# Performance work log

Measured on AMD Instinct MI355X. Metric: run time of the kernel, lower is better.

The kernel has to match this reference:

```python
import jax, jax.numpy as jnp
import numpy as np

S, L, B = 64, 64, 16
D_IN, D_ATTN = 1024, 512


def setup_inputs() -> dict:
    key = jax.random.key(0)
    ks = jax.random.split(key, 8)
    context = jax.random.normal(ks[0], (S, L, B, D_IN), dtype=jnp.float32)
    query = jax.random.normal(ks[1], (L, B, D_IN), dtype=jnp.float32)
    mask = jnp.ones((S, L, B), dtype=jnp.int32)
    # Linear params (torch layout: weight [out, in], bias [out])
    sc = 1.0 / np.sqrt(D_IN)
    Wc = jax.random.uniform(ks[2], (D_ATTN, D_IN), minval=-sc, maxval=sc, dtype=jnp.float32)
    bc = jax.random.uniform(ks[3], (D_ATTN,), minval=-sc, maxval=sc, dtype=jnp.float32)
    Wq = jax.random.uniform(ks[4], (D_ATTN, D_IN), minval=-sc, maxval=sc, dtype=jnp.float32)
    bq = jax.random.uniform(ks[5], (D_ATTN,), minval=-sc, maxval=sc, dtype=jnp.float32)
    v = jax.random.uniform(ks[6], (D_ATTN,), dtype=jnp.float32)  # torch.rand -> U[0,1)
    return {"context": context, "query": query, "mask": mask,
            "Wc": Wc, "bc": bc, "Wq": Wq, "bq": bq, "v": v}


def reference(context, query, mask, Wc, bc, Wq, bq, v):
    # context: [s,l,b,din], query: [l,b,din]
    context_proj = jnp.einsum('slbi,di->slbd', context, Wc) + bc  # [s,l,b,da]
    query_proj = jnp.einsum('lbi,di->lbd', query, Wq) + bq        # [l,b,da]
    scores = jnp.tanh(context_proj + query_proj[None])            # [s,l,b,da]
    scores = jnp.einsum('slbd,d->slb', scores, v)                 # [s,l,b]
    scores = jnp.where(mask == 0, jnp.float32(-1e9), scores)
    alpha = jax.nn.softmax(scores, axis=0)                        # softmax over s
    attn_output = jnp.einsum('slb,slbd->lbd', alpha, context)     # [l,b,din]
    return (attn_output, alpha)
```

## Files before the change

kernel.cpp:

```cpp
#include <hip/hip_runtime.h>
#include <hip/hip_fp16.h>
#include <stdint.h>

#define S_DIM 64
#define L_DIM 64
#define B_DIM 16
#define LB    1024
#define DIN   1024
#define DA    512
#define M_TOT 65536

#define BM 128
#define BN 512
#define BK 64
#define NT (DIN / BK)

using f16x8 = __attribute__((ext_vector_type(8))) _Float16;
using f32x4 = __attribute__((ext_vector_type(4))) float;

typedef const __attribute__((address_space(1))) void* gas_ptr;
typedef __attribute__((address_space(3))) void* las_ptr;

__device__ __forceinline__ void load_lds16(const void* g, void* l) {
    __builtin_amdgcn_global_load_lds((gas_ptr)g, (las_ptr)l, 16, 0, 0);
}

__device__ __forceinline__ float fast_tanh(float x) {
    return 1.0f - 2.0f / (__expf(2.0f * x) + 1.0f);
}

__global__ void cvt_all(const float* __restrict__ Wc, const float* __restrict__ Wq,
                        const float* __restrict__ q,
                        _Float16* __restrict__ Wch, _Float16* __restrict__ Wqh,
                        _Float16* __restrict__ Qh) {
    int i = blockIdx.x * 256 + threadIdx.x;
    if (i < DA * DIN)            Wch[i] = (_Float16)Wc[i];
    else if (i < 2 * DA * DIN)   Wqh[i - DA * DIN] = (_Float16)Wq[i - DA * DIN];
    else                         Qh[i - 2 * DA * DIN] = (_Float16)q[i - 2 * DA * DIN];
}

__global__ __launch_bounds__(256) void qp_gemm(
    const _Float16* __restrict__ Qh,
    const _Float16* __restrict__ Wqh,
    const float* __restrict__ bq, const float* __restrict__ bc,
    float* __restrict__ qp)
{
    __shared__ __align__(16) _Float16 lA[64 * 64];
    __shared__ __align__(16) _Float16 lB[64 * 64];
    const int t = threadIdx.x;
    const int w = t >> 6, lane = t & 63;
    const int quad = lane >> 4, m16 = lane & 15;
    const int n0 = blockIdx.x * 64, lb0 = blockIdx.y * 64;

    f32x4 acc[4] = {};

    for (int kt = 0; kt < DIN / 64; ++kt) {
#pragma unroll
        for (int i = 0; i < 2; ++i) {
            int c = (w * 2 + i) * 64 + lane;
            int row = c >> 3;
            int kc = (c & 7) ^ (row & 7);
            load_lds16(Qh  + (size_t)(lb0 + row) * DIN + kt * 64 + kc * 8, (char*)lA + (size_t)c * 16);
            load_lds16(Wqh + (size_t)(n0  + row) * DIN + kt * 64 + kc * 8, (char*)lB + (size_t)c * 16);
        }
        __syncthreads();
#pragma unroll
        for (int kk = 0; kk < 64; kk += 32) {
            int cq = (kk >> 3) + quad;
            int ar = 16 * w + m16;
            f16x8 a = *(const f16x8*)((const char*)lA + ar * 128 + ((cq ^ (ar & 7)) * 16));
#pragma unroll
            for (int j = 0; j < 4; ++j) {
                int br = 16 * j + m16;
                f16x8 b = *(const f16x8*)((const char*)lB + br * 128 + ((cq ^ (br & 7)) * 16));
                acc[j] = __builtin_amdgcn_mfma_f32_16x16x32_f16(a, b, acc[j], 0, 0, 0);
            }
        }
        __syncthreads();
    }
#pragma unroll
    for (int j = 0; j < 4; ++j) {
        int n = n0 + 16 * j + m16;
        float bias = bq[n] + bc[n];
#pragma unroll
        for (int r = 0; r < 4; ++r) {
            int lb = lb0 + 16 * w + quad * 4 + r;
            qp[(size_t)lb * DA + n] = acc[j][r] + bias;
        }
    }
}

__global__ __launch_bounds__(512, 2) void score_gemm4(
    const float* __restrict__ ctx,
    const _Float16* __restrict__ Wch,
    const float* __restrict__ qp,
    const float* __restrict__ v,
    _Float16* __restrict__ ctxh,
    float* __restrict__ sc)
{
    __shared__ __align__(16) _Float16 lA[BM * BK];
    __shared__ __align__(16) _Float16 lB[2][BN * BK];
    __shared__ float lP[4][BM];

    const int t = threadIdx.x;
    const int w = t >> 6, lane = t & 63;
    const int quad = lane >> 4, m16 = lane & 15;
    const int wm = w & 1, wn = w >> 1;

    int bid = blockIdx.x;
    int mb = (bid & 7) * 64 + (bid >> 3);
    const int m0 = mb * BM;
    const int lb0 = m0 & (LB - 1);

    const int arow = t >> 2;
    const int c0   = (t & 3) * 2;

    auto stageB = [&](int kt, int buf) {
#pragma unroll
        for (int i = 0; i < 8; ++i) {
            int c = (w * 8 + i) * 64 + lane;
            int row = c >> 3;
            int kc = (c & 7) ^ (row & 7);
            load_lds16(Wch + (size_t)row * DIN + kt * BK + kc * 8,
                       (char*)lB[buf] + (size_t)c * 16);
        }
    };

    f32x4 pf[4];
    auto issueA = [&](int kt) {
        const float* p = ctx + (size_t)(m0 + arow) * DIN + kt * BK + c0 * 8;
        pf[0] = *(const f32x4*)(p);
        pf[1] = *(const f32x4*)(p + 4);
        pf[2] = *(const f32x4*)(p + 8);
        pf[3] = *(const f32x4*)(p + 12);
    };

    stageB(0, 0);
    issueA(0);

    f32x4 acc[4][8];
#pragma unroll
    for (int i = 0; i < 4; ++i) {
        int rl = lb0 + wm * 64 + 16 * i + quad * 4;
#pragma unroll
        for (int j = 0; j < 8; ++j) {
            int n = wn * 128 + 16 * j + m16;
#pragma unroll
            for (int r = 0; r < 4; ++r)
                acc[i][j][r] = qp[(size_t)(rl + r) * DA + n];
        }
    }

    asm volatile("s_waitcnt vmcnt(0)" ::: "memory");
    __builtin_amdgcn_s_barrier();
    __builtin_amdgcn_sched_barrier(0);

    for (int kt = 0; kt < NT; ++kt) {
        const int cur = kt & 1;

        f16x8 h0 = {(_Float16)pf[0][0], (_Float16)pf[0][1], (_Float16)pf[0][2], (_Float16)pf[0][3],
                    (_Float16)pf[1][0], (_Float16)pf[1][1], (_Float16)pf[1][2], (_Float16)pf[1][3]};
        f16x8 h1 = {(_Float16)pf[2][0], (_Float16)pf[2][1], (_Float16)pf[2][2], (_Float16)pf[2][3],
                    (_Float16)pf[3][0], (_Float16)pf[3][1], (_Float16)pf[3][2], (_Float16)pf[3][3]};
        *(f16x8*)((char*)lA + arow * 128 + (((c0)     ^ (arow & 7)) * 16)) = h0;
        *(f16x8*)((char*)lA + arow * 128 + (((c0 + 1) ^ (arow & 7)) * 16)) = h1;
        _Float16* cd = ctxh + (size_t)(m0 + arow) * DIN + kt * BK + c0 * 8;
        *(f16x8*)cd = h0;
        *(f16x8*)(cd + 8) = h1;

        if (kt + 1 < NT) { stageB(kt + 1, cur ^ 1); issueA(kt + 1); }

        asm volatile("s_waitcnt lgkmcnt(0)" ::: "memory");
        __builtin_amdgcn_s_barrier();
        __builtin_amdgcn_sched_barrier(0);

#pragma unroll
        for (int kk2 = 0; kk2 < 2; ++kk2) {
            int cq = kk2 * 4 + quad;
            f16x8 a[4], b[8];
#pragma unroll
            for (int i = 0; i < 4; ++i) {
                int ar = wm * 64 + 16 * i + m16;
                a[i] = *(const f16x8*)((const char*)lA + ar * 128 + ((cq ^ (ar & 7)) * 16));
            }
#pragma unroll
            for (int j = 0; j < 8; ++j) {
                int br = wn * 128 + 16 * j + m16;
                b[j] = *(const f16x8*)((const char*)lB[cur] + br * 128 + ((cq ^ (br & 7)) * 16));
            }
            __builtin_amdgcn_s_setprio(1);
#pragma unroll
            for (int i = 0; i < 4; ++i)
#pragma unroll
                for (int j = 0; j < 8; ++j)
                    acc[i][j] = __builtin_amdgcn_mfma_f32_16x16x32_f16(a[i], b[j], acc[i][j], 0, 0, 0);
            __builtin_amdgcn_s_setprio(0);
        }

        asm volatile("s_waitcnt vmcnt(0)" ::: "memory");
        __builtin_amdgcn_s_barrier();
        __builtin_amdgcn_sched_barrier(0);
    }

    float vv[8];
#pragma unroll
    for (int j = 0; j < 8; ++j) vv[j] = v[wn * 128 + 16 * j + m16];

    float part[16];
#pragma unroll
    for (int i = 0; i < 4; ++i)
#pragma unroll
        for (int r = 0; r < 4; ++r) {
            float s = 0.f;
#pragma unroll
            for (int j = 0; j < 8; ++j)
                s += fast_tanh(acc[i][j][r]) * vv[j];
            part[i * 4 + r] = s;
        }
#pragma unroll
    for (int off = 1; off < 16; off <<= 1) {
#pragma unroll
        for (int k = 0; k < 16; ++k) part[k] += __shfl_xor(part[k], off, 64);
    }
    if (m16 == 0) {
#pragma unroll
        for (int k = 0; k < 16; ++k) {
            int rl = wm * 64 + 16 * (k >> 2) + quad * 4 + (k & 3);
            lP[wn][rl] = part[k];
        }
    }
    __syncthreads();
    if (t < BM) {
        float s = lP[0][t] + lP[1][t] + lP[2][t] + lP[3][t];
        sc[m0 + t] = s;
    }
}

__global__ __launch_bounds__(256, 3) void score_gemm(
    const float* __restrict__ ctx, const _Float16* __restrict__ Wch,
    const float* __restrict__ qp, const float* __restrict__ v,
    float* __restrict__ scores)
{
    __shared__ __align__(16) _Float16 lA[128 * 64];
    __shared__ __align__(16) _Float16 lB[128 * 64];
    __shared__ float lP[2][128];

    const int t = threadIdx.x;
    const int w = t >> 6, lane = t & 63;
    const int quad = lane >> 4, m16 = lane & 15;
    const int wm = w & 1, wn = w >> 1;

    int bid = blockIdx.x;
    int xcd = bid & 7;
    int j2 = bid >> 3;
    int nqf = j2 & 3;
    int mbf = ((j2 >> 2) << 3) | xcd;
    const int m0 = mbf * 128;
    const int n0 = nqf * 128;

    f32x4 acc[4][4] = {};

    const int arow = t >> 1;
    const int akc4 = (t & 1) * 4;
    const float* gA = ctx + (size_t)(m0 + arow) * DIN + (t & 1) * 32;

    for (int kt = 0; kt < DIN / 64; ++kt) {
        {
            const float* p = gA + kt * 64;
            f32x4 f[8];
#pragma unroll
            for (int qd = 0; qd < 8; ++qd) f[qd] = *(const f32x4*)(p + qd * 4);
#pragma unroll
            for (int q2 = 0; q2 < 4; ++q2) {
                f16x8 h = {(_Float16)f[2*q2][0], (_Float16)f[2*q2][1],
                           (_Float16)f[2*q2][2], (_Float16)f[2*q2][3],
                           (_Float16)f[2*q2+1][0], (_Float16)f[2*q2+1][1],
                           (_Float16)f[2*q2+1][2], (_Float16)f[2*q2+1][3]};
                int c = akc4 + q2;
                *(f16x8*)((char*)lA + arow * 128 + ((c ^ (arow & 7)) * 16)) = h;
            }
        }
#pragma unroll
        for (int i = 0; i < 4; ++i) {
            int c = (w * 4 + i) * 64 + lane;
            int row = c >> 3;
            int kc = (c & 7) ^ (row & 7);
            load_lds16(Wch + (size_t)(n0 + row) * DIN + kt * 64 + kc * 8, (char*)lB + (size_t)c * 16);
        }
        __syncthreads();
#pragma unroll
        for (int kk = 0; kk < 64; kk += 32) {
            int cq = (kk >> 3) + quad;
            f16x8 a[4], b[4];
#pragma unroll
            for (int i = 0; i < 4; ++i) {
                int ar = wm * 64 + 16 * i + m16;
                a[i] = *(const f16x8*)((const char*)lA + ar * 128 + ((cq ^ (ar & 7)) * 16));
            }
#pragma unroll
            for (int j = 0; j < 4; ++j) {
                int br = wn * 64 + 16 * j + m16;
                b[j] = *(const f16x8*)((const char*)lB + br * 128 + ((cq ^ (br & 7)) * 16));
            }
#pragma unroll
            for (int i = 0; i < 4; ++i)
#pragma unroll
                for (int j = 0; j < 4; ++j)
                    acc[i][j] = __builtin_amdgcn_mfma_f32_16x16x32_f16(a[i], b[j], acc[i][j], 0, 0, 0);
        }
        __syncthreads();
    }

    float vv[4];
    int nn[4];
#pragma unroll
    for (int j = 0; j < 4; ++j) { nn[j] = n0 + wn * 64 + 16 * j + m16; vv[j] = v[nn[j]]; }

    float part[16];
#pragma unroll
    for (int i = 0; i < 4; ++i) {
#pragma unroll
        for (int r = 0; r < 4; ++r) {
            int gm = m0 + wm * 64 + 16 * i + quad * 4 + r;
            int lb = gm & (LB - 1);
            float s = 0.f;
#pragma unroll
            for (int j = 0; j < 4; ++j) {
                float x = acc[i][j][r] + qp[(size_t)lb * DA + nn[j]];
                s += fast_tanh(x) * vv[j];
            }
            part[i * 4 + r] = s;
        }
    }
#pragma unroll
    for (int off = 1; off < 16; off <<= 1) {
#pragma unroll
        for (int k = 0; k < 16; ++k) part[k] += __shfl_xor(part[k], off, 64);
    }
    if (m16 == 0) {
#pragma unroll
        for (int k = 0; k < 16; ++k) {
            int row_local = wm * 64 + 16 * (k >> 2) + quad * 4 + (k & 3);
            lP[wn][row_local] = part[k];
        }
    }
    __syncthreads();
    if (t < 128) {
        float s = lP[0][t] + lP[1][t];
        atomicAdd(&scores[m0 + t], s);
    }
}

__global__ __launch_bounds__(64) void softmax2(const float* __restrict__ scores,
                                               const int* __restrict__ mask,
                                               float* __restrict__ alpha) {
    int lb = blockIdx.x;
    int s = threadIdx.x;
    float x = scores[s * LB + lb];
    if (mask[s * LB + lb] == 0) x = -1e9f;
    float mx = x;
#pragma unroll
    for (int off = 1; off < 64; off <<= 1) mx = fmaxf(mx, __shfl_xor(mx, off, 64));
    float e = __expf(x - mx);
    float sum = e;
#pragma unroll
    for (int off = 1; off < 64; off <<= 1) sum += __shfl_xor(sum, off, 64);
    alpha[s * LB + lb] = e / sum;
}

__global__ __launch_bounds__(128) void weighted_sum2(
    const _Float16* __restrict__ ctxh, const float* __restrict__ alpha,
    float* __restrict__ out) {
    __shared__ float lAl[S_DIM];
    const int lb = blockIdx.x;
    const int t = threadIdx.x;
    if (t < S_DIM) lAl[t] = alpha[t * LB + lb];
    __syncthreads();
    float acc[8] = {};
    const _Float16* base = ctxh + (size_t)lb * DIN + t * 8;
#pragma unroll 8
    for (int s = 0; s < S_DIM; ++s) {
        float a = lAl[s];
        f16x8 c = *(const f16x8*)(base + (size_t)s * LB * DIN);
#pragma unroll
        for (int j = 0; j < 8; ++j) acc[j] += a * (float)c[j];
    }
    f32x4 lo = {acc[0], acc[1], acc[2], acc[3]};
    f32x4 hi = {acc[4], acc[5], acc[6], acc[7]};
    *(f32x4*)(out + (size_t)lb * DIN + t * 8) = lo;
    *(f32x4*)(out + (size_t)lb * DIN + t * 8 + 4) = hi;
}

__global__ __launch_bounds__(256) void weighted_sum(
    const float* __restrict__ ctx, const float* __restrict__ alpha,
    float* __restrict__ out) {
    __shared__ float lAl[S_DIM];
    const int lb = blockIdx.x;
    const int t = threadIdx.x;
    if (t < S_DIM) lAl[t] = alpha[t * LB + lb];
    __syncthreads();
    f32x4 acc = {0.f, 0.f, 0.f, 0.f};
    const float* base = ctx + (size_t)lb * DIN + t * 4;
#pragma unroll 4
    for (int s = 0; s < S_DIM; ++s) {
        float a = lAl[s];
        f32x4 c = *(const f32x4*)(base + (size_t)s * LB * DIN);
        acc += a * c;
    }
    *(f32x4*)(out + (size_t)lb * DIN + t * 4) = acc;
}

extern "C" void kernel_launch(void* const* d_in, const int* in_sizes, int n_in,
                              void* d_out, int out_size, void* d_ws, size_t ws_size,
                              hipStream_t stream) {
    (void)in_sizes; (void)n_in; (void)out_size;
    const float* ctx   = (const float*)d_in[0];
    const float* query = (const float*)d_in[1];
    const int*   mask  = (const int*)d_in[2];
    const float* Wc    = (const float*)d_in[3];
    const float* bc    = (const float*)d_in[4];
    const float* Wq    = (const float*)d_in[5];
    const float* bq    = (const float*)d_in[6];
    const float* v     = (const float*)d_in[7];

    float* out_attn  = (float*)d_out;
    float* out_alpha = (float*)d_out + (size_t)LB * DIN;

    char* ws = (char*)d_ws;
    _Float16* Wch = (_Float16*)(ws);
    _Float16* Wqh = (_Float16*)(ws + (1 << 20));
    _Float16* Qh  = (_Float16*)(ws + (2 << 20));
    float*    qp  = (float*)(ws + (4 << 20));
    float*    sc  = (float*)(ws + (6 << 20));
    _Float16* ctxh = (_Float16*)(ws + (8 << 20));

    const size_t need = (size_t)(8 + 128) << 20;
    const bool bigws = ws_size >= need;

    cvt_all<<<(2 * DA * DIN + LB * DIN) / 256, 256, 0, stream>>>(Wc, Wq, query, Wch, Wqh, Qh);
    qp_gemm<<<dim3(DA / 64, LB / 64), 256, 0, stream>>>(Qh, Wqh, bq, bc, qp);

    if (bigws) {
        score_gemm4<<<M_TOT / BM, 512, 0, stream>>>(ctx, Wch, qp, v, ctxh, sc);
        softmax2<<<LB, 64, 0, stream>>>(sc, mask, out_alpha);
        weighted_sum2<<<LB, 128, 0, stream>>>(ctxh, out_alpha, out_attn);
    } else {
        hipMemsetAsync(sc, 0, (size_t)M_TOT * sizeof(float), stream);
        score_gemm<<<2048, 256, 0, stream>>>(ctx, Wch, qp, v, sc);
        softmax2<<<LB, 64, 0, stream>>>(sc, mask, out_alpha);
        weighted_sum<<<LB, 256, 0, stream>>>(ctx, out_alpha, out_attn);
    }
}
```

Measured before the change: 483.4 us.

## Split score GEMM across two N-halves with single-buffered B for higher occupancy

The fused score GEMM now tiles N at 256 instead of 512, so each block handles half of the attention dimension and the grid doubles. It writes two partial score arrays that a new softmax kernel sums. B is single-buffered and loaded each iteration, with vmcnt-based waits replacing the full drain, and launch bounds request more waves per CU. Only one of each block pair writes the fp16 context copy. The cost is that the context A tile is read and converted twice, and the B load is no longer prefetched a step ahead, which may expose latency.

```diff
diff --git a/kernel.cpp b/kernel.cpp
--- a/kernel.cpp
+++ b/kernel.cpp
@@ -11,7 +11,7 @@
 #define M_TOT 65536
 
 #define BM 128
-#define BN 512
+#define BN 256
 #define BK 64
 #define NT (DIN / BK)
 
@@ -90,7 +90,7 @@
     }
 }
 
-__global__ __launch_bounds__(512, 2) void score_gemm4(
+__global__ __launch_bounds__(512, 6) void score_gemm5(
     const float* __restrict__ ctx,
     const _Float16* __restrict__ Wch,
     const float* __restrict__ qp,
@@ -99,7 +99,7 @@
     float* __restrict__ sc)
 {
     __shared__ __align__(16) _Float16 lA[BM * BK];
-    __shared__ __align__(16) _Float16 lB[2][BN * BK];
+    __shared__ __align__(16) _Float16 lB[BN * BK];
     __shared__ float lP[4][BM];
 
     const int t = threadIdx.x;
@@ -108,21 +108,26 @@
     const int wm = w & 1, wn = w >> 1;
 
     int bid = blockIdx.x;
-    int mb = (bid & 7) * 64 + (bid >> 3);
+    int xcd = bid & 7;
+    int idx = bid >> 3;
+    const int nq = idx & 1;
+    const int mb = xcd * 64 + (idx >> 1);
     const int m0 = mb * BM;
+    const int n0 = nq * BN;
     const int lb0 = m0 & (LB - 1);
+    const bool wr_ctxh = (nq == 0);
 
     const int arow = t >> 2;
     const int c0   = (t & 3) * 2;
 
-    auto stageB = [&](int kt, int buf) {
-#pragma unroll
-        for (int i = 0; i < 8; ++i) {
-            int c = (w * 8 + i) * 64 + lane;
+    auto stageB = [&](int kt) {
+#pragma unroll
+        for (int i = 0; i < 4; ++i) {
+            int c = (w * 4 + i) * 64 + lane;
             int row = c >> 3;
             int kc = (c & 7) ^ (row & 7);
-            load_lds16(Wch + (size_t)row * DIN + kt * BK + kc * 8,
-                       (char*)lB[buf] + (size_t)c * 16);
+            load_lds16(Wch + (size_t)(n0 + row) * DIN + kt * BK + kc * 8,
+                       (char*)lB + (size_t)c * 16);
         }
     };
 
@@ -135,28 +140,23 @@
         pf[3] = *(const f32x4*)(p + 12);
     };
 
-    stageB(0, 0);
     issueA(0);
 
-    f32x4 acc[4][8];
+    f32x4 acc[4][4];
 #pragma unroll
     for (int i = 0; i < 4; ++i) {
         int rl = lb0 + wm * 64 + 16 * i + quad * 4;
 #pragma unroll
-        for (int j = 0; j < 8; ++j) {
-            int n = wn * 128 + 16 * j + m16;
+        for (int j = 0; j < 4; ++j) {
+            int n = n0 + wn * 64 + 16 * j + m16;
 #pragma unroll
             for (int r = 0; r < 4; ++r)
                 acc[i][j][r] = qp[(size_t)(rl + r) * DA + n];
         }
     }
 
-    asm volatile("s_waitcnt vmcnt(0)" ::: "memory");
-    __builtin_amdgcn_s_barrier();
-    __builtin_amdgcn_sched_barrier(0);
-
     for (int kt = 0; kt < NT; ++kt) {
-        const int cur = kt & 1;
+        stageB(kt);
 
         f16x8 h0 = {(_Float16)pf[0][0], (_Float16)pf[0][1], (_Float16)pf[0][2], (_Float16)pf[0][3],
                     (_Float16)pf[1][0], (_Float16)pf[1][1], (_Float16)pf[1][2], (_Float16)pf[1][3]};
@@ -164,12 +164,16 @@
                     (_Float16)pf[3][0], (_Float16)pf[3][1], (_Float16)pf[3][2], (_Float16)pf[3][3]};
         *(f16x8*)((char*)lA + arow * 128 + (((c0)     ^ (arow & 7)) * 16)) = h0;
         *(f16x8*)((char*)lA + arow * 128 + (((c0 + 1) ^ (arow & 7)) * 16)) = h1;
-        _Float16* cd = ctxh + (size_t)(m0 + arow) * DIN + kt * BK + c0 * 8;
-        *(f16x8*)cd = h0;
-        *(f16x8*)(cd + 8) = h1;
-
-        if (kt + 1 < NT) { stageB(kt + 1, cur ^ 1); issueA(kt + 1); }
-
+        if (wr_ctxh) {
+            _Float16* cd = ctxh + (size_t)(m0 + arow) * DIN + kt * BK + c0 * 8;
+            *(f16x8*)cd = h0;
+            *(f16x8*)(cd + 8) = h1;
+        }
+
+        issueA(kt + 1 < NT ? kt + 1 : NT - 1);
+
+        if (wr_ctxh) asm volatile("s_waitcnt vmcnt(6)" ::: "memory");
+        else         asm volatile("s_waitcnt vmcnt(4)" ::: "memory");
         asm volatile("s_waitcnt lgkmcnt(0)" ::: "memory");
         __builtin_amdgcn_s_barrier();
         __builtin_amdgcn_sched_barrier(0);
@@ -177,34 +181,34 @@
 #pragma unroll
         for (int kk2 = 0; kk2 < 2; ++kk2) {
             int cq = kk2 * 4 + quad;
-            f16x8 a[4], b[8];
+            f16x8 a[4], b[4];
 #pragma unroll
             for (int i = 0; i < 4; ++i) {
                 int ar = wm * 64 + 16 * i + m16;
                 a[i] = *(const f16x8*)((const char*)lA + ar * 128 + ((cq ^ (ar & 7)) * 16));
             }
 #pragma unroll
-            for (int j = 0; j < 8; ++j) {
-                int br = wn * 128 + 16 * j + m16;
-                b[j] = *(const f16x8*)((const char*)lB[cur] + br * 128 + ((cq ^ (br & 7)) * 16));
+            for (int j = 0; j < 4; ++j) {
+                int br = wn * 64 + 16 * j + m16;
+                b[j] = *(const f16x8*)((const char*)lB + br * 128 + ((cq ^ (br & 7)) * 16));
             }
             __builtin_amdgcn_s_setprio(1);
 #pragma unroll
             for (int i = 0; i < 4; ++i)
 #pragma unroll
-                for (int j = 0; j < 8; ++j)
+                for (int j = 0; j < 4; ++j)
                     acc[i][j] = __builtin_amdgcn_mfma_f32_16x16x32_f16(a[i], b[j], acc[i][j], 0, 0, 0);
             __builtin_amdgcn_s_setprio(0);
         }
 
-        asm volatile("s_waitcnt vmcnt(0)" ::: "memory");
+        __builtin_amdgcn_sched_barrier(0);
         __builtin_amdgcn_s_barrier();
         __builtin_amdgcn_sched_barrier(0);
     }
 
-    float vv[8];
-#pragma unroll
-    for (int j = 0; j < 8; ++j) vv[j] = v[wn * 128 + 16 * j + m16];
+    float vv[4];
+#pragma unroll
+    for (int j = 0; j < 4; ++j) vv[j] = v[n0 + wn * 64 + 16 * j + m16];
 
     float part[16];
 #pragma unroll
@@ -213,7 +217,7 @@
         for (int r = 0; r < 4; ++r) {
             float s = 0.f;
 #pragma unroll
-            for (int j = 0; j < 8; ++j)
+            for (int j = 0; j < 4; ++j)
                 s += fast_tanh(acc[i][j][r]) * vv[j];
             part[i * 4 + r] = s;
         }
@@ -232,7 +236,7 @@
     __syncthreads();
     if (t < BM) {
         float s = lP[0][t] + lP[1][t] + lP[2][t] + lP[3][t];
-        sc[m0 + t] = s;
+        sc[(size_t)nq * M_TOT + m0 + t] = s;
     }
 }
 
@@ -349,6 +353,24 @@
         float s = lP[0][t] + lP[1][t];
         atomicAdd(&scores[m0 + t], s);
     }
+}
+
+__global__ __launch_bounds__(64) void softmax3(const float* __restrict__ sc,
+                                               const int* __restrict__ mask,
+                                               float* __restrict__ alpha) {
+    int lb = blockIdx.x;
+    int s = threadIdx.x;
+    int m = s * LB + lb;
+    float x = sc[m] + sc[M_TOT + m];
+    if (mask[m] == 0) x = -1e9f;
+    float mx = x;
+#pragma unroll
+    for (int off = 1; off < 64; off <<= 1) mx = fmaxf(mx, __shfl_xor(mx, off, 64));
+    float e = __expf(x - mx);
+    float sum = e;
+#pragma unroll
+    for (int off = 1; off < 64; off <<= 1) sum += __shfl_xor(sum, off, 64);
+    alpha[m] = e / sum;
 }
 
 __global__ __launch_bounds__(64) void softmax2(const float* __restrict__ scores,
@@ -441,8 +463,8 @@
     qp_gemm<<<dim3(DA / 64, LB / 64), 256, 0, stream>>>(Qh, Wqh, bq, bc, qp);
 
     if (bigws) {
-        score_gemm4<<<M_TOT / BM, 512, 0, stream>>>(ctx, Wch, qp, v, ctxh, sc);
-        softmax2<<<LB, 64, 0, stream>>>(sc, mask, out_alpha);
+        score_gemm5<<<(M_TOT / BM) * (DA / BN), 512, 0, stream>>>(ctx, Wch, qp, v, ctxh, sc);
+        softmax3<<<LB, 64, 0, stream>>>(sc, mask, out_alpha);
         weighted_sum2<<<LB, 128, 0, stream>>>(ctxh, out_alpha, out_attn);
     } else {
         hipMemsetAsync(sc, 0, (size_t)M_TOT * sizeof(float), stream);
```

After: 1.373 ms. 184% more time.
